# Optimization experiments

Measured on AMD Instinct MI355X. Metric: run time of the kernel, lower is better.

Reference implementation:

```python
import math
import jax, jax.numpy as jnp
import numpy as np

B, H, L, D = 32, 8, 4096, 64
FACTOR = 5


def setup_inputs() -> dict:
    key = jax.random.key(0)
    kq, kk, kv, ki = jax.random.split(key, 4)
    U_part = min(FACTOR * int(math.ceil(math.log(L))), L)  # 45
    return {
        "queries": jax.random.normal(kq, (B, H, L, D), jnp.float32),
        "keys": jax.random.normal(kk, (B, H, L, D), jnp.float32),
        "values": jax.random.normal(kv, (B, H, L, D), jnp.float32),
        "index_sample": jax.random.randint(ki, (L, U_part), 0, L),
        "attn_mask": jnp.ones((1,), bool),  # presence flag only
    }


def reference(queries, keys, values, index_sample, attn_mask):
    Bq, Hq, L_Q, Dd = queries.shape
    L_K = keys.shape[2]
    u = min(FACTOR * int(math.ceil(math.log(L_Q))), L_Q)
    scale = 1.0 / math.sqrt(Dd)

    # --- _prob_QK: sample K columns per query, score sparsity measure M ---
    K_sample = jnp.take(keys, index_sample, axis=2)            # [B,H,L_Q,sample_k,D]
    Q_K_sample = jnp.einsum('bhqd,bhqkd->bhqk', queries, K_sample)
    M = Q_K_sample.max(axis=-1) - Q_K_sample.mean(axis=-1)     # [B,H,L_Q]
    M_top = jnp.argsort(M, axis=-1)[:, :, -u:]                 # [B,H,u]
    Q_reduce = jnp.take_along_axis(queries, M_top[..., None], axis=2)  # [B,H,u,D]
    scores = jnp.einsum('bhqd,bhkd->bhqk', Q_reduce, keys) * scale      # [B,H,u,L_K]

    # --- ProbMask (mask_flag=True, attn_mask present): causal mask gathered at M_top ---
    causal = jnp.triu(jnp.ones((L_Q, L_K), dtype=bool), k=1)   # [L_Q,L_K]
    mask = causal[M_top]                                       # [B,H,u,L_K]
    scores = jnp.where(mask, -jnp.inf, scores)

    attn = jax.nn.softmax(scores, axis=-1)                     # [B,H,u,L_K]

    # --- initial context: cumulative sum of V (causal mean surrogate) ---
    context = jnp.cumsum(values, axis=2)                       # [B,H,L_Q,D]

    # --- scatter the attended values at the selected top-u query positions ---
    bi = jnp.arange(Bq)[:, None, None]
    hi = jnp.arange(Hq)[None, :, None]
    upd = jnp.einsum('bhqk,bhkd->bhqd', attn, values)          # [B,H,u,D]
    context = context.at[bi, hi, M_top].set(upd)

    return jnp.transpose(context, (0, 2, 1, 3))                # [B,L_Q,H,D]
```

## Files before the change

kernel.cpp:

```cpp
#include <hip/hip_runtime.h>
#include <hip/hip_bf16.h>

#define B_  32
#define H_  8
#define L_  4096
#define D_  64
#define BH_ 256
#define U_  45
#define UP_ 48

#define CHUNK_R 256
#define NCH     16
#define QCH     1024
#define NQC     4
#define NCELLS  1024
#define NENT    (L_ * U_)

typedef float f32x4  __attribute__((ext_vector_type(4)));
typedef float f32x2  __attribute__((ext_vector_type(2)));
typedef short bf16x8 __attribute__((ext_vector_type(8)));

__device__ __forceinline__ unsigned short f2bf(float f) {
  unsigned u = __builtin_bit_cast(unsigned, f);
  u += 0x7fffu + ((u >> 16) & 1u);
  return (unsigned short)(u >> 16);
}

__global__ __launch_bounds__(1024) void k_prep(
    const int* __restrict__ idxg, unsigned* __restrict__ cellbase,
    unsigned* __restrict__ entries)
{
  __shared__ unsigned cnt[NCELLS];
  const int t = threadIdx.x;
  cnt[t] = 0u;
  __syncthreads();
  for (int i = t; i < NENT; i += 1024) {
    const int q = i / U_;
    const int v = idxg[i];
    const int cell = ((v >> 8) << 6) | (q >> 6);
    atomicAdd(&cnt[cell], 1u);
  }
  __syncthreads();
  if (t == 0) {
    unsigned run = 0;
    for (int c = 0; c < NCELLS; c++) { cellbase[c] = run; run += cnt[c]; }
    cellbase[NCELLS] = run;
  }
  __syncthreads();
  cnt[t] = cellbase[t];
  __syncthreads();
  for (int i = t; i < NENT; i += 1024) {
    const int q = i / U_;
    const int v = idxg[i];
    const int cell = ((v >> 8) << 6) | (q >> 6);
    const unsigned slot = atomicAdd(&cnt[cell], 1u);
    entries[slot] = ((unsigned)q << 8) | (unsigned)(v & 255);
  }
}

__global__ __launch_bounds__(1024) void k_probM(
    const float* __restrict__ Qg, const float* __restrict__ Kg,
    const unsigned* __restrict__ cellbase, const unsigned* __restrict__ entries,
    float* __restrict__ Mg)
{
  const int bid = blockIdx.x;
  const int xcd = bid & 7, kk = bid >> 3;
  const int bh  = xcd + ((kk >> 2) << 3);
  const int qc  = kk & 3;

  __shared__ float kbuf[2][CHUNK_R * 64];
  __shared__ int                smax[QCH];
  __shared__ unsigned long long ssum[QCH];

  const int t = threadIdx.x;
  smax[t] = (int)0x80000000;
  ssum[t] = 0ull;

  const float* Kb = Kg + (size_t)bh * (L_ * D_);

#define STAGE(KC, BSEL) do { \
    _Pragma("unroll") \
    for (int uu = 0; uu < 4; uu++) { \
      const int l_  = t + uu * 1024; \
      const int r_  = l_ >> 4, p_ = l_ & 15; \
      const int us_ = p_ ^ (r_ & 15); \
      const float* src_ = Kb + ((size_t)((KC) * CHUNK_R + r_)) * 64 + us_ * 4; \
      __builtin_amdgcn_global_load_lds( \
          (const __attribute__((address_space(1))) void*)src_, \
          (__attribute__((address_space(3))) void*)(&kbuf[BSEL][0] + l_ * 4), \
          16, 0, 0); \
    } \
  } while (0)

  STAGE(0, 0);
  __syncthreads();

  const int quad = t >> 2, lq = t & 3;
  const int qf0  = qc * 16;

  for (int kc = 0; kc < NCH; kc++) {
    const int cur = kc & 1;
    if (kc + 1 < NCH) STAGE(kc + 1, cur ^ 1);

    const unsigned e0 = cellbase[(kc << 6) + qf0];
    const unsigned e1 = cellbase[(kc << 6) + qf0 + 16];

    for (unsigned e = e0 + quad; e < e1; e += 256) {
      const unsigned ent = entries[e];
      const int q = (int)(ent >> 8);
      const int r = (int)(ent & 255u);

      const float* qp = Qg + ((size_t)bh * L_ + q) * 64 + lq * 16;
      const f32x4 qa = *(const f32x4*)(qp);
      const f32x4 qb = *(const f32x4*)(qp + 4);
      const f32x4 qcv= *(const f32x4*)(qp + 8);
      const f32x4 qd = *(const f32x4*)(qp + 12);

      const float* kb0 = &kbuf[cur][r * 64];
      const int rx = r & 15;
      const int u0 = (lq * 4 + 0) ^ rx;
      const int u1 = (lq * 4 + 1) ^ rx;
      const int u2 = (lq * 4 + 2) ^ rx;
      const int u3 = (lq * 4 + 3) ^ rx;
      const f32x2 k0a = *(const f32x2*)(kb0 + u0 * 4);
      const f32x2 k0b = *(const f32x2*)(kb0 + u0 * 4 + 2);
      const f32x2 k1a = *(const f32x2*)(kb0 + u1 * 4);
      const f32x2 k1b = *(const f32x2*)(kb0 + u1 * 4 + 2);
      const f32x2 k2a = *(const f32x2*)(kb0 + u2 * 4);
      const f32x2 k2b = *(const f32x2*)(kb0 + u2 * 4 + 2);
      const f32x2 k3a = *(const f32x2*)(kb0 + u3 * 4);
      const f32x2 k3b = *(const f32x2*)(kb0 + u3 * 4 + 2);

      float d0 = 0.f, d1 = 0.f;
      d0 = fmaf(qa[0], k0a[0], d0); d1 = fmaf(qa[1], k0a[1], d1);
      d0 = fmaf(qa[2], k0b[0], d0); d1 = fmaf(qa[3], k0b[1], d1);
      d0 = fmaf(qb[0], k1a[0], d0); d1 = fmaf(qb[1], k1a[1], d1);
      d0 = fmaf(qb[2], k1b[0], d0); d1 = fmaf(qb[3], k1b[1], d1);
      d0 = fmaf(qcv[0], k2a[0], d0); d1 = fmaf(qcv[1], k2a[1], d1);
      d0 = fmaf(qcv[2], k2b[0], d0); d1 = fmaf(qcv[3], k2b[1], d1);
      d0 = fmaf(qd[0], k3a[0], d0); d1 = fmaf(qd[1], k3a[1], d1);
      d0 = fmaf(qd[2], k3b[0], d0); d1 = fmaf(qd[3], k3b[1], d1);
      float dot = d0 + d1;
      dot += __shfl_xor(dot, 1);
      dot += __shfl_xor(dot, 2);

      if (lq == 0) {
        const int fx = (int)rintf(dot * 1048576.0f);
        atomicMax(&smax[q & (QCH - 1)], fx);
        atomicAdd(&ssum[q & (QCH - 1)], (unsigned long long)(long long)fx);
      }
    }
    __syncthreads();
  }
#undef STAGE

  {
    const double inv = 1.0 / 1048576.0;
    const double mx = (double)smax[t] * inv;
    const double sm = (double)(long long)ssum[t] * inv;
    Mg[(size_t)bh * L_ + qc * QCH + t] = (float)(mx - sm / 45.0);
  }
}

__global__ __launch_bounds__(256) void k_top45(
    const float* __restrict__ Mg, int* __restrict__ qselg)
{
  __shared__ float mv[L_];
  __shared__ float rv[256];
  __shared__ int   ri[256];
  __shared__ int   sels[UP_];
  const int bh = blockIdx.x, t = threadIdx.x;

  for (int i = t; i < L_; i += 256) mv[i] = Mg[(size_t)bh * L_ + i];
  __syncthreads();

  for (int it = 0; it < U_; it++) {
    float bv = -3.4e38f; int bi = 0;
    for (int i = t; i < L_; i += 256) {
      float v = mv[i];
      if (v > bv) { bv = v; bi = i; }
    }
    rv[t] = bv; ri[t] = bi;
    __syncthreads();
    for (int s = 128; s > 0; s >>= 1) {
      if (t < s) {
        float ov = rv[t + s];
        if (ov > rv[t] || (ov == rv[t] && ri[t + s] < ri[t])) {
          rv[t] = ov; ri[t] = ri[t + s];
        }
      }
      __syncthreads();
    }
    if (t == 0) { sels[it] = ri[0]; mv[ri[0]] = -3.4e38f; }
    __syncthreads();
  }
  if (t == 0) { sels[45] = sels[0]; sels[46] = sels[0]; sels[47] = sels[0]; }
  __syncthreads();
  if (t < UP_) qselg[bh * UP_ + t] = sels[t];
}

__global__ __launch_bounds__(512) void k_cumsum(
    const float* __restrict__ Vg, float* __restrict__ out)
{
  const int bh = blockIdx.x, b = bh >> 3, h = bh & 7;
  const int d = threadIdx.x & 63, s = threadIdx.x >> 6;
  __shared__ float segsum[8][64];

  const float* vb = Vg + (size_t)bh * L_ * D_ + d;
  const int l0 = s * 512;

  float acc = 0.f;
  for (int l = l0; l < l0 + 512; l += 4) {
    float a0 = vb[(size_t)(l + 0) * D_];
    float a1 = vb[(size_t)(l + 1) * D_];
    float a2 = vb[(size_t)(l + 2) * D_];
    float a3 = vb[(size_t)(l + 3) * D_];
    acc += a0; acc += a1; acc += a2; acc += a3;
  }
  segsum[s][d] = acc;
  __syncthreads();

  float run = 0.f;
  for (int ss = 0; ss < s; ss++) run += segsum[ss][d];

  float* ob = out + ((size_t)b * L_ * H_ + h) * D_ + d;
  for (int l = l0; l < l0 + 512; l += 4) {
    float a0 = vb[(size_t)(l + 0) * D_];
    float a1 = vb[(size_t)(l + 1) * D_];
    float a2 = vb[(size_t)(l + 2) * D_];
    float a3 = vb[(size_t)(l + 3) * D_];
    run += a0; ob[(size_t)(l + 0) * (H_ * D_)] = run;
    run += a1; ob[(size_t)(l + 1) * (H_ * D_)] = run;
    run += a2; ob[(size_t)(l + 2) * (H_ * D_)] = run;
    run += a3; ob[(size_t)(l + 3) * (H_ * D_)] = run;
  }
}

__global__ __launch_bounds__(512, 2) void k_attn(
    const float* __restrict__ Qg, const float* __restrict__ Kg,
    const float* __restrict__ Vg, const int* __restrict__ qselg,
    float* __restrict__ out)
{
  const int bh = blockIdx.x, b = bh >> 3, h = bh & 7;
  const int wave = threadIdx.x >> 6, lane = threadIdx.x & 63;
  const int l15 = lane & 15, l4 = lane >> 4;

  __shared__ int   qs[UP_];
  __shared__ float mw[8][UP_];
  __shared__ float lw[8][UP_];
  __shared__ float lgf[UP_];
  __shared__ float Osum[UP_][64];
  __shared__ unsigned short Pl[8][16][72];

  if (threadIdx.x < UP_) qs[threadIdx.x] = qselg[bh * UP_ + threadIdx.x];
  for (int i = threadIdx.x; i < UP_ * 64; i += 512) (&Osum[0][0])[i] = 0.f;
  __syncthreads();

  int qmax = 0;
  for (int r2 = 0; r2 < UP_; r2++) qmax = max(qmax, qs[r2]);

  const float* Qb = Qg + (size_t)bh * L_ * D_;
  const float* Kb = Kg + (size_t)bh * L_ * D_;
  const float* Vb = Vg + (size_t)bh * L_ * D_;

  bf16x8 aq[3][2];
#pragma unroll
  for (int mf = 0; mf < 3; mf++) {
    const float* src = Qb + (size_t)qs[mf * 16 + l15] * D_ + l4 * 8;
#pragma unroll
    for (int ks = 0; ks < 2; ks++) {
      bf16x8 a;
#pragma unroll
      for (int j = 0; j < 8; j++) a[j] = (short)f2bf(src[ks * 32 + j]);
      aq[mf][ks] = a;
    }
  }

  int myq[3][4];
#pragma unroll
  for (int mf = 0; mf < 3; mf++)
#pragma unroll
    for (int rg = 0; rg < 4; rg++)
      myq[mf][rg] = qs[mf * 16 + l4 * 4 + rg];

  float m_r[3][4], l_r[3][4];
  f32x4 Oa[3][4];
  const f32x4 z4 = {0.f, 0.f, 0.f, 0.f};
#pragma unroll
  for (int mf = 0; mf < 3; mf++)
#pragma unroll
    for (int rg = 0; rg < 4; rg++) { m_r[mf][rg] = -1e30f; l_r[mf][rg] = 0.f; }
#pragma unroll
  for (int mf = 0; mf < 3; mf++)
#pragma unroll
    for (int df = 0; df < 4; df++) Oa[mf][df] = z4;

  for (int t = 0; t < 8; t++) {
    const int k0 = wave * 512 + t * 64;
    if (k0 > qmax) break;

    f32x4 S[3][4];
#pragma unroll
    for (int nf = 0; nf < 4; nf++) {
      const float* ksrc = Kb + (size_t)(k0 + nf * 16 + l15) * D_ + l4 * 8;
      bf16x8 bk0, bk1;
#pragma unroll
      for (int j = 0; j < 8; j++) bk0[j] = (short)f2bf(ksrc[j]);
#pragma unroll
      for (int j = 0; j < 8; j++) bk1[j] = (short)f2bf(ksrc[32 + j]);
#pragma unroll
      for (int mf = 0; mf < 3; mf++) {
        f32x4 c = z4;
        c = __builtin_amdgcn_mfma_f32_16x16x32_bf16(aq[mf][0], bk0, c, 0, 0, 0);
        c = __builtin_amdgcn_mfma_f32_16x16x32_bf16(aq[mf][1], bk1, c, 0, 0, 0);
        S[mf][nf] = c;
      }
    }

#pragma unroll
    for (int mf = 0; mf < 3; mf++)
#pragma unroll
      for (int nf = 0; nf < 4; nf++) {
        const int kc = k0 + nf * 16 + l15;
#pragma unroll
        for (int rg = 0; rg < 4; rg++) {
          float v = S[mf][nf][rg] * 0.125f;
          S[mf][nf][rg] = (kc > myq[mf][rg]) ? -1e30f : v;
        }
      }

    bf16x8 vv[2][4];
#pragma unroll
    for (int ks = 0; ks < 2; ks++)
#pragma unroll
      for (int df = 0; df < 4; df++) {
        bf16x8 x;
#pragma unroll
        for (int j = 0; j < 8; j++)
          x[j] = (short)f2bf(Vb[(size_t)(k0 + ks * 32 + l4 * 8 + j) * D_ + df * 16 + l15]);
        vv[ks][df] = x;
      }

#pragma unroll
    for (int mf = 0; mf < 3; mf++) {
#pragma unroll
      for (int rg = 0; rg < 4; rg++) {
        float tm = fmax(fmax(S[mf][0][rg], S[mf][1][rg]),
                        fmax(S[mf][2][rg], S[mf][3][rg]));
#pragma unroll
        for (int off = 1; off < 16; off <<= 1) tm = fmax(tm, __shfl_xor(tm, off));
        const float mn = fmax(m_r[mf][rg], tm);
        const float sc = __expf(m_r[mf][rg] - mn);
        l_r[mf][rg] *= sc;
#pragma unroll
        for (int df = 0; df < 4; df++) Oa[mf][df][rg] *= sc;
        m_r[mf][rg] = mn;
      }

      float rs[4] = {0.f, 0.f, 0.f, 0.f};
#pragma unroll
      for (int nf = 0; nf < 4; nf++)
#pragma unroll
        for (int rg = 0; rg < 4; rg++) {
          float p = __expf(S[mf][nf][rg] - m_r[mf][rg]);
          p = (m_r[mf][rg] > -1e29f) ? p : 0.f;
          rs[rg] += p;
          Pl[wave][l4 * 4 + rg][nf * 16 + l15] = f2bf(p);
        }
#pragma unroll
      for (int rg = 0; rg < 4; rg++) {
        float r = rs[rg];
#pragma unroll
        for (int off = 1; off < 16; off <<= 1) r += __shfl_xor(r, off);
        l_r[mf][rg] += r;
      }

#pragma unroll
      for (int ks = 0; ks < 2; ks++) {
        const bf16x8 pa = *(const bf16x8*)(&Pl[wave][l15][ks * 32 + l4 * 8]);
#pragma unroll
        for (int df = 0; df < 4; df++)
          Oa[mf][df] = __builtin_amdgcn_mfma_f32_16x16x32_bf16(pa, vv[ks][df], Oa[mf][df], 0, 0, 0);
      }
    }
  }

  if (l15 == 0) {
#pragma unroll
    for (int mf = 0; mf < 3; mf++)
#pragma unroll
      for (int rg = 0; rg < 4; rg++) {
        const int row = mf * 16 + l4 * 4 + rg;
        mw[wave][row] = m_r[mf][rg];
        lw[wave][row] = l_r[mf][rg];
      }
  }
  __syncthreads();

  float sc_me[3][4];
#pragma unroll
  for (int mf = 0; mf < 3; mf++)
#pragma unroll
    for (int rg = 0; rg < 4; rg++) {
      const int row = mf * 16 + l4 * 4 + rg;
      float m = -1e30f;
#pragma unroll
      for (int w = 0; w < 8; w++) m = fmax(m, mw[w][row]);
      float ls = 0.f;
#pragma unroll
      for (int w = 0; w < 8; w++) ls += lw[w][row] * __expf(mw[w][row] - m);
      sc_me[mf][rg] = __expf(m_r[mf][rg] - m);
      if (wave == 0 && l15 == 0) lgf[row] = ls;
    }

  for (int w = 0; w < 8; w++) {
    __syncthreads();
    if (wave == w) {
#pragma unroll
      for (int mf = 0; mf < 3; mf++)
#pragma unroll
        for (int df = 0; df < 4; df++)
#pragma unroll
          for (int rg = 0; rg < 4; rg++)
            Osum[mf * 16 + l4 * 4 + rg][df * 16 + l15] += Oa[mf][df][rg] * sc_me[mf][rg];
    }
  }
  __syncthreads();

  for (int i = threadIdx.x; i < U_ * 64; i += 512) {
    const int r = i >> 6, d = i & 63;
    out[(((size_t)b * L_ + (size_t)qs[r]) * H_ + h) * D_ + d] = Osum[r][d] / lgf[r];
  }
}

extern "C" void kernel_launch(void* const* d_in, const int* in_sizes, int n_in,
                              void* d_out, int out_size, void* d_ws, size_t ws_size,
                              hipStream_t stream)
{
  const float* Q   = (const float*)d_in[0];
  const float* K   = (const float*)d_in[1];
  const float* V   = (const float*)d_in[2];
  const int*   idx = (const int*)d_in[3];
  float* out = (float*)d_out;

  const size_t m_bytes    = (size_t)BH_ * L_ * sizeof(float);
  const size_t qsel_bytes = (size_t)BH_ * UP_ * sizeof(int);
  const size_t ent_bytes  = (size_t)NENT * sizeof(unsigned);
  const size_t cb_bytes   = (size_t)(NCELLS + 1) * sizeof(unsigned);

  char* p = (char*)d_ws;
  float*    M        = (float*)p;                 p += m_bytes;
  int*      qsel     = (int*)p;                   p += qsel_bytes;
  unsigned* entries  = (unsigned*)p;              p += ent_bytes;
  unsigned* cellbase = (unsigned*)p;              p += cb_bytes;
  if (ws_size < (size_t)(p - (char*)d_ws)) return;

  k_prep  <<<1,    1024, 0, stream>>>(idx, cellbase, entries);
  k_probM <<<1024, 1024, 0, stream>>>(Q, K, cellbase, entries, M);
  k_top45 <<<BH_,  256,  0, stream>>>(M, qsel);
  k_cumsum<<<BH_,  512,  0, stream>>>(V, out);
  k_attn  <<<BH_,  512,  0, stream>>>(Q, K, V, qsel, out);
}
```

Measured before the change: 1.472 ms.

## Parallelize bucket prep across blocks, halve K chunk size, prefetch entries

The single-block bucketing kernel is split into three launches: a global-atomic count over 64 blocks, a one-block prefix scan, and a 64-block fill. K chunks in the probM kernel shrink from 256 to 128 rows, which doubles the cell count and halves LDS use per buffer, possibly improving occupancy. The entry loop also software-prefetches the next entry index. The trade-offs are more launches, global atomic contention, and twice as many chunk iterations with their barriers.

```diff
diff --git a/kernel.cpp b/kernel.cpp
--- a/kernel.cpp
+++ b/kernel.cpp
@@ -9,11 +9,10 @@
 #define U_  45
 #define UP_ 48
 
-#define CHUNK_R 256
-#define NCH     16
+#define CHUNK_R 128
+#define NCH     32
 #define QCH     1024
-#define NQC     4
-#define NCELLS  1024
+#define NCELLS  2048
 #define NENT    (L_ * U_)
 
 typedef float f32x4  __attribute__((ext_vector_type(4)));
@@ -26,35 +25,42 @@
   return (unsigned short)(u >> 16);
 }
 
-__global__ __launch_bounds__(1024) void k_prep(
-    const int* __restrict__ idxg, unsigned* __restrict__ cellbase,
-    unsigned* __restrict__ entries)
-{
-  __shared__ unsigned cnt[NCELLS];
-  const int t = threadIdx.x;
-  cnt[t] = 0u;
-  __syncthreads();
-  for (int i = t; i < NENT; i += 1024) {
+__global__ __launch_bounds__(1024) void k_pcount(
+    const int* __restrict__ idxg, unsigned* __restrict__ gcnt)
+{
+  for (int i = blockIdx.x * 1024 + threadIdx.x; i < NENT; i += 64 * 1024) {
     const int q = i / U_;
     const int v = idxg[i];
-    const int cell = ((v >> 8) << 6) | (q >> 6);
-    atomicAdd(&cnt[cell], 1u);
-  }
+    atomicAdd(&gcnt[((v >> 7) << 6) | (q >> 6)], 1u);
+  }
+}
+
+__global__ __launch_bounds__(1024) void k_pscan(
+    const unsigned* __restrict__ gcnt, unsigned* __restrict__ cellbase,
+    unsigned* __restrict__ gcur)
+{
+  __shared__ unsigned v[NCELLS];
+  const int t = threadIdx.x;
+  v[t] = gcnt[t]; v[t + 1024] = gcnt[t + 1024];
   __syncthreads();
   if (t == 0) {
     unsigned run = 0;
-    for (int c = 0; c < NCELLS; c++) { cellbase[c] = run; run += cnt[c]; }
+    for (int c = 0; c < NCELLS; c++) {
+      cellbase[c] = run; gcur[c] = run; run += v[c];
+    }
     cellbase[NCELLS] = run;
   }
-  __syncthreads();
-  cnt[t] = cellbase[t];
-  __syncthreads();
-  for (int i = t; i < NENT; i += 1024) {
+}
+
+__global__ __launch_bounds__(1024) void k_pfill(
+    const int* __restrict__ idxg, unsigned* __restrict__ gcur,
+    unsigned* __restrict__ entries)
+{
+  for (int i = blockIdx.x * 1024 + threadIdx.x; i < NENT; i += 64 * 1024) {
     const int q = i / U_;
     const int v = idxg[i];
-    const int cell = ((v >> 8) << 6) | (q >> 6);
-    const unsigned slot = atomicAdd(&cnt[cell], 1u);
-    entries[slot] = ((unsigned)q << 8) | (unsigned)(v & 255);
+    const unsigned slot = atomicAdd(&gcur[((v >> 7) << 6) | (q >> 6)], 1u);
+    entries[slot] = ((unsigned)q << 8) | (unsigned)(v & 127);
   }
 }
 
@@ -80,7 +86,7 @@
 
 #define STAGE(KC, BSEL) do { \
     _Pragma("unroll") \
-    for (int uu = 0; uu < 4; uu++) { \
+    for (int uu = 0; uu < 2; uu++) { \
       const int l_  = t + uu * 1024; \
       const int r_  = l_ >> 4, p_ = l_ & 15; \
       const int us_ = p_ ^ (r_ & 15); \
@@ -105,10 +111,16 @@
     const unsigned e0 = cellbase[(kc << 6) + qf0];
     const unsigned e1 = cellbase[(kc << 6) + qf0 + 16];
 
-    for (unsigned e = e0 + quad; e < e1; e += 256) {
-      const unsigned ent = entries[e];
+    unsigned e    = e0 + quad;
+    bool     have = e < e1;
+    unsigned ent  = have ? entries[e] : 0u;
+    while (have) {
+      const unsigned e2    = e + 256;
+      const bool     have2 = e2 < e1;
+      const unsigned ent2  = have2 ? entries[e2] : 0u;
+
       const int q = (int)(ent >> 8);
-      const int r = (int)(ent & 255u);
+      const int r = (int)(ent & 127u);
 
       const float* qp = Qg + ((size_t)bh * L_ + q) * 64 + lq * 16;
       const f32x4 qa = *(const f32x4*)(qp);
@@ -149,6 +161,8 @@
         atomicMax(&smax[q & (QCH - 1)], fx);
         atomicAdd(&ssum[q & (QCH - 1)], (unsigned long long)(long long)fx);
       }
+
+      e = e2; ent = ent2; have = have2;
     }
     __syncthreads();
   }
@@ -447,15 +461,21 @@
   const size_t qsel_bytes = (size_t)BH_ * UP_ * sizeof(int);
   const size_t ent_bytes  = (size_t)NENT * sizeof(unsigned);
   const size_t cb_bytes   = (size_t)(NCELLS + 1) * sizeof(unsigned);
+  const size_t cnt_bytes  = (size_t)NCELLS * sizeof(unsigned);
 
   char* p = (char*)d_ws;
   float*    M        = (float*)p;                 p += m_bytes;
   int*      qsel     = (int*)p;                   p += qsel_bytes;
   unsigned* entries  = (unsigned*)p;              p += ent_bytes;
   unsigned* cellbase = (unsigned*)p;              p += cb_bytes;
+  unsigned* gcnt     = (unsigned*)p;              p += cnt_bytes;
+  unsigned* gcur     = (unsigned*)p;              p += cnt_bytes;
   if (ws_size < (size_t)(p - (char*)d_ws)) return;
 
-  k_prep  <<<1,    1024, 0, stream>>>(idx, cellbase, entries);
+  hipMemsetAsync(gcnt, 0, cnt_bytes, stream);
+  k_pcount<<<64,   1024, 0, stream>>>(idx, gcnt);
+  k_pscan <<<1,    1024, 0, stream>>>(gcnt, cellbase, gcur);
+  k_pfill <<<64,   1024, 0, stream>>>(idx, gcur, entries);
   k_probM <<<1024, 1024, 0, stream>>>(Q, K, cellbase, entries, M);
   k_top45 <<<BH_,  256,  0, stream>>>(M, qsel);
   k_cumsum<<<BH_,  512,  0, stream>>>(V, out);
```

Measured after the change: 1.439 ms. 2.3% less time.
